# Performance work log

Measured on AMD Instinct MI355X. Metric: run time of the kernel, lower is better.

The kernel has to match this reference:

```python
import jax, jax.numpy as jnp
import numpy as np

N, E, B, L = 500000, 1500000, 64, 512
H, C_IN, C_CONV = 64, 2, 64


def setup_inputs() -> dict:
    key = jax.random.key(0)
    ks = jax.random.split(key, 12)
    x = jax.random.normal(ks[0], (N, C_IN), jnp.float32)
    edge_index = jax.random.randint(ks[1], (2, E), 0, N)
    node_depth = jax.random.randint(ks[2], (N,), 0, L)
    batch_index = jnp.sort(jax.random.randint(ks[3], (N,), 0, B))
    W1 = jax.random.normal(ks[4], (C_IN, H), jnp.float32) / np.sqrt(C_IN)
    b1 = jnp.zeros((H,), jnp.float32)
    W2 = jax.random.normal(ks[5], (H, H), jnp.float32) / np.sqrt(H)
    b2 = jnp.zeros((H,), jnp.float32)
    conv_w = jax.random.normal(ks[6], (C_CONV, 2 * H, 3), jnp.float32) / np.sqrt(2 * H * 3)
    conv_b = jnp.zeros((C_CONV,), jnp.float32)
    fc1_w = jax.random.normal(ks[7], (C_CONV, C_CONV), jnp.float32) / np.sqrt(C_CONV)
    fc1_b = jnp.zeros((C_CONV,), jnp.float32)
    fc2_w = jax.random.normal(ks[8], (C_CONV, 1), jnp.float32) / np.sqrt(C_CONV)
    fc2_b = jnp.zeros((1,), jnp.float32)
    return {"x": x, "edge_index": edge_index, "node_depth": node_depth,
            "batch_index": batch_index, "W1": W1, "b1": b1, "W2": W2, "b2": b2,
            "conv_w": conv_w, "conv_b": conv_b, "fc1_w": fc1_w, "fc1_b": fc1_b,
            "fc2_w": fc2_w, "fc2_b": fc2_b}


def _gcn(x, W, b, src, dst):
    # PyG GCNConv: add self-loops, D^{-1/2} (A+I) D^{-1/2} X W + b
    xw = x @ W
    deg = jnp.zeros((N,), xw.dtype).at[dst].add(1.0) + 1.0  # +1 for self-loop
    dinv = jax.lax.rsqrt(deg)
    norm = dinv[src] * dinv[dst]  # [E]
    agg = jnp.zeros_like(xw).at[dst].add(norm[:, None] * xw[src])
    agg = agg + (dinv * dinv)[:, None] * xw  # self-loop term
    return agg + b


def reference(x, edge_index, node_depth, batch_index, W1, b1, W2, b2,
              conv_w, conv_b, fc1_w, fc1_b, fc2_w, fc2_b):
    src, dst = edge_index[0], edge_index[1]
    h = jax.nn.relu(_gcn(x, W1, b1, src, dst))
    h = jax.nn.relu(_gcn(h, W2, b2, src, dst))

    # LevelWisePool: grouped mean+max keyed by (batch, depth)
    seg = batch_index * L + node_depth  # [N]
    cnt = jax.ops.segment_sum(jnp.ones((N,), h.dtype), seg, num_segments=B * L)
    mean = jax.ops.segment_sum(h, seg, num_segments=B * L) / jnp.maximum(cnt, 1.0)[:, None]
    mx = jax.ops.segment_max(h, seg, num_segments=B * L)
    mx = jnp.where(cnt[:, None] > 0, mx, 0.0)  # empty levels -> zeros
    seq = jnp.concatenate([mean, mx], axis=-1)           # [B*L, 2H]
    seq = seq.reshape(B, L, 2 * H).transpose(0, 2, 1)    # [B, 2H, L]

    y = jax.lax.conv_general_dilated(seq, conv_w, window_strides=(1,),
                                     padding=[(1, 1)],
                                     dimension_numbers=("NCH", "OIH", "NCH"))
    y = jax.nn.relu(y + conv_b[None, :, None])  # [B, C_CONV, L]
    pooled = y.mean(axis=2)                      # [B, C_CONV]

    z = jax.nn.relu(pooled @ fc1_w + fc1_b)
    logits = (z @ fc2_w + fc2_b).reshape(-1)     # [B]
    return jax.nn.sigmoid(logits)
```

## Files before the change

### kernel.cpp

```cpp
#include <hip/hip_runtime.h>

typedef unsigned short ushort_t;
typedef unsigned int uint_t;
typedef __attribute__((ext_vector_type(8))) short short8;
typedef __attribute__((ext_vector_type(4))) float f32x4;

#define NN 500000
#define NE 1500000
#define BATCH 64
#define LSEQ 512
#define NSEG (BATCH * LSEQ)
#define NBLK_E ((NN + 1023) / 1024)
#define NBLK_S (NSEG / 1024)
#define SEQROW 514
#define WPKN (3 * 4 * 4 * 512)
#define PSMASK 0x7FFFFu

__device__ inline float bf2f(ushort_t u) {
    union { uint_t u; float f; } c; c.u = ((uint_t)u) << 16; return c.f;
}
__device__ inline ushort_t f2bf(float f) {
    union { float f; uint_t u; } c; c.f = f;
    uint_t u = c.u;
    return (ushort_t)((u + 0x7fff + ((u >> 16) & 1)) >> 16);
}
__device__ inline int imax(int a, int b) { return a > b ? a : b; }

__global__ void k_zero(float* __restrict__ p, int n) {
    int i = blockIdx.x * blockDim.x + threadIdx.x;
    int stride = gridDim.x * blockDim.x;
    for (; i < n; i += stride) p[i] = 0.0f;
}

__global__ void k_hist2(const int* __restrict__ dst, const int* __restrict__ batch,
                        const int* __restrict__ depth, int* __restrict__ cnt,
                        int* __restrict__ segn, int* __restrict__ cnt2) {
    int t = blockIdx.x * blockDim.x + threadIdx.x;
    if (t < NE) {
        atomicAdd(&cnt[dst[t]], 1);
        if (t < NN) {
            int s = batch[t] * LSEQ + depth[t];
            segn[t] = s;
            atomicAdd(&cnt2[s], 1);
        }
    }
}

__global__ __launch_bounds__(256) void k_scan_block(const int* __restrict__ cnt,
                                                    int* __restrict__ bsum, int n) {
    __shared__ int sd[256];
    int blk = blockIdx.x, tid = threadIdx.x;
    int base = blk * 1024 + tid * 4;
    int s = 0;
#pragma unroll
    for (int k = 0; k < 4; ++k) { int i = base + k; if (i < n) s += cnt[i]; }
    sd[tid] = s;
    __syncthreads();
    for (int off = 128; off; off >>= 1) {
        if (tid < off) sd[tid] += sd[tid + off];
        __syncthreads();
    }
    if (tid == 0) bsum[blk] = sd[0];
}

__global__ __launch_bounds__(512) void k_scan_top(int* __restrict__ bsum, int nblk) {
    __shared__ int sd[512];
    int tid = threadIdx.x;
    int v = (tid < nblk) ? bsum[tid] : 0;
    sd[tid] = v;
    __syncthreads();
    for (int off = 1; off < 512; off <<= 1) {
        int t = (tid >= off) ? sd[tid - off] : 0;
        __syncthreads();
        sd[tid] += t;
        __syncthreads();
    }
    if (tid < nblk) bsum[tid] = sd[tid] - v;
}

__global__ __launch_bounds__(256) void k_scan_final(const int* __restrict__ cnt, const int* __restrict__ bsum,
                                                    int* __restrict__ rowoff, int* __restrict__ cursor,
                                                    int n, int total) {
    __shared__ int sd[256];
    int blk = blockIdx.x, tid = threadIdx.x;
    int base = blk * 1024 + tid * 4;
    int loc[4]; int s = 0;
#pragma unroll
    for (int k = 0; k < 4; ++k) { int i = base + k; int c = (i < n) ? cnt[i] : 0; loc[k] = s; s += c; }
    sd[tid] = s;
    __syncthreads();
    for (int off = 1; off < 256; off <<= 1) {
        int t = (tid >= off) ? sd[tid - off] : 0;
        __syncthreads();
        sd[tid] += t;
        __syncthreads();
    }
    int texc = sd[tid] - s + bsum[blk];
#pragma unroll
    for (int k = 0; k < 4; ++k) {
        int i = base + k;
        if (i < n) { int v = texc + loc[k]; rowoff[i] = v; cursor[i] = v; }
    }
    if (blk == 0 && tid == 0) rowoff[n] = total;
}

__global__ void k_nreorder(const int* __restrict__ segn, int* __restrict__ cursor2,
                           int* __restrict__ nord, int* __restrict__ pos) {
    int n = blockIdx.x * blockDim.x + threadIdx.x;
    if (n >= NN) return;
    int p = atomicAdd(&cursor2[segn[n]], 1);
    nord[p] = n;
    pos[n] = p;
}

__global__ void k_prep(const int* __restrict__ cnt, const int* __restrict__ nord,
                       float* __restrict__ dinvs, int* __restrict__ cntp,
                       const float* __restrict__ x, float2* __restrict__ xs,
                       const float* __restrict__ W2, ushort_t* __restrict__ W2b,
                       const float* __restrict__ cw, ushort_t* __restrict__ wpk) {
    int i = blockIdx.x * blockDim.x + threadIdx.x;
    if (i < NN) {
        int nd = nord[i];
        int dg = cnt[nd];
        cntp[i] = dg;
        float dv = rsqrtf((float)dg + 1.0f);
        dinvs[i] = dv;
        const float2* x2 = (const float2*)x;
        float2 xv = x2[nd];
        xs[i] = make_float2(dv * xv.x, dv * xv.y);
    }
    if (i < 64 * 64) W2b[i] = f2bf(W2[i]);
    if (i < WPKN) {
        int bq = i & 7, ln = (i >> 3) & 63, ct = (i >> 9) & 3, kk = (i >> 11) & 3, tap = i >> 13;
        int c = ct * 16 + (ln & 15);
        int ii = kk * 32 + (ln >> 4) * 8 + bq;
        wpk[i] = f2bf(cw[c * 384 + ii * 3 + tap]);
    }
}

__global__ void k_reorder(const int* __restrict__ src, const int* __restrict__ dst,
                          const int* __restrict__ pos,
                          int* __restrict__ cursor, uint_t* __restrict__ epr) {
    int e = blockIdx.x * blockDim.x + threadIdx.x;
    if (e >= NE) return;
    int ps = pos[src[e]], pd = pos[dst[e]];
    int q = atomicAdd(&cursor[pd], 1);
    epr[q] = (uint_t)ps | ((uint_t)(pd & 15) << 19);
}

__global__ __launch_bounds__(256) void k_build12(const float2* __restrict__ xs,
                                                 const float* __restrict__ W1,
                                                 const float* __restrict__ b1,
                                                 const float* __restrict__ dinvs,
                                                 const int* __restrict__ rowoff,
                                                 const uint_t* __restrict__ epr,
                                                 const ushort_t* __restrict__ W2b,
                                                 ushort_t* __restrict__ xw2) {
    __shared__ float accs[4][32];
    __shared__ ushort_t hl[4][16][64];
    int lane = threadIdx.x & 63;
    int wid = threadIdx.x >> 6;
    int wave = (blockIdx.x * blockDim.x + threadIdx.x) >> 6;
    int nwaves = (gridDim.x * blockDim.x) >> 6;
    int col = lane & 15, kg = lane >> 4;
    float w0 = W1[lane], w1 = W1[64 + lane], bj = b1[lane];
    float* a = accs[wid];
    ushort_t (*h)[64] = hl[wid];
    const float* xsf = (const float*)xs;

    short8 bfrag[2][4];
#pragma unroll
    for (int t = 0; t < 2; ++t)
#pragma unroll
        for (int j = 0; j < 4; ++j)
#pragma unroll
            for (int b = 0; b < 8; ++b) {
                int k = t * 32 + kg * 8 + b;
                bfrag[t][j][b] = (short)W2b[k * 64 + j * 16 + col];
            }

    int kblk = lane >> 3, kin = lane & 7;
    const int NT = NN / 16;
    for (int t = wave; t < NT; t += nwaves) {
        int i0 = t * 16;
        if (lane < 32) a[lane] = xsf[i0 * 2 + lane];
        asm volatile("s_waitcnt lgkmcnt(0)" ::: "memory");
        int e1 = rowoff[i0 + 16];
        for (int e = rowoff[i0] + lane; e < e1; e += 64) {
            uint_t pr = epr[e];
            float2 xv = xs[pr & PSMASK];
            int loc = (pr >> 19) & 15;
            atomicAdd(&a[loc * 2],     xv.x);
            atomicAdd(&a[loc * 2 + 1], xv.y);
        }
        asm volatile("s_waitcnt lgkmcnt(0)" ::: "memory");
#pragma unroll
        for (int j = 0; j < 16; ++j) {
            float dv = dinvs[i0 + j];
            float hv = fmaxf((dv * a[j * 2]) * w0 + (dv * a[j * 2 + 1]) * w1 + bj, 0.0f);
            h[j][((kblk ^ (j & 7)) << 3) + kin] = f2bf(hv);
        }
        asm volatile("s_waitcnt lgkmcnt(0)" ::: "memory");
        short8 a0 = *(const short8*)&h[col][((kg ^ (col & 7)) << 3)];
        short8 a1 = *(const short8*)&h[col][(((kg + 4) ^ (col & 7)) << 3)];
        float dvr[4];
#pragma unroll
        for (int r = 0; r < 4; ++r) dvr[r] = dinvs[i0 + kg * 4 + r];
        size_t base = (size_t)i0 * 64;
        f32x4 acc[4];
#pragma unroll
        for (int j = 0; j < 4; ++j) {
            acc[j] = (f32x4){0.0f, 0.0f, 0.0f, 0.0f};
            acc[j] = __builtin_amdgcn_mfma_f32_16x16x32_bf16(a0, bfrag[0][j], acc[j], 0, 0, 0);
            acc[j] = __builtin_amdgcn_mfma_f32_16x16x32_bf16(a1, bfrag[1][j], acc[j], 0, 0, 0);
        }
#pragma unroll
        for (int j = 0; j < 4; ++j)
#pragma unroll
            for (int r = 0; r < 4; ++r)
                xw2[base + (size_t)(kg * 4 + r) * 64 + j * 16 + col] = f2bf(acc[j][r] * dvr[r]);
    }
}

__global__ __launch_bounds__(256) void k_agg3(const ushort_t* __restrict__ xw2s,
                                              const float* __restrict__ b2,
                                              const float* __restrict__ dinvs,
                                              const int* __restrict__ rowoff,
                                              const uint_t* __restrict__ epr,
                                              ushort_t* __restrict__ aggs) {
    __shared__ float accs[4][16][64];
    int lane = threadIdx.x & 63;
    int wid = threadIdx.x >> 6;
    int wave = (blockIdx.x * blockDim.x + threadIdx.x) >> 6;
    int nwaves = (gridDim.x * blockDim.x) >> 6;
    float bj = b2[lane];
    float (*a)[64] = accs[wid];
    const int NT = NN / 16;
    for (int t = wave; t < NT; t += nwaves) {
        int i0 = t * 16;
#pragma unroll
        for (int j = 0; j < 16; ++j)
            a[j][lane] = bf2f(xw2s[(size_t)(i0 + j) * 64 + lane]);
        int e = rowoff[i0], e1 = rowoff[i0 + 16];
        for (; e + 8 <= e1; e += 8) {
            uint_t p[8];
#pragma unroll
            for (int jj = 0; jj < 8; ++jj) p[jj] = epr[e + jj];
            float v[8];
#pragma unroll
            for (int jj = 0; jj < 8; ++jj)
                v[jj] = bf2f(xw2s[(size_t)(p[jj] & PSMASK) * 64 + lane]);
#pragma unroll
            for (int jj = 0; jj < 8; ++jj)
                a[(p[jj] >> 19) & 15][lane] += v[jj];
        }
        for (; e < e1; ++e) {
            uint_t p = epr[e];
            a[(p >> 19) & 15][lane] += bf2f(xw2s[(size_t)(p & PSMASK) * 64 + lane]);
        }
#pragma unroll
        for (int j = 0; j < 16; ++j) {
            float dv = dinvs[i0 + j];
            aggs[(size_t)(i0 + j) * 64 + lane] = f2bf(fmaxf(dv * a[j][lane] + bj, 0.0f));
        }
    }
}

__global__ __launch_bounds__(256) void k_pool2(const ushort_t* __restrict__ aggs,
                                               const int* __restrict__ soff,
                                               ushort_t* __restrict__ seqb) {
    int lane = threadIdx.x & 63;
    int seg = (blockIdx.x * blockDim.x + threadIdx.x) >> 6;
    if (seg >= NSEG) return;
    int i0 = soff[seg], i1 = soff[seg + 1];
    float ss = 0.0f, sm = 0.0f;
    for (int i = i0; i < i1; ++i) {
        float v = bf2f(aggs[(size_t)i * 64 + lane]);
        ss += v;
        sm = fmaxf(sm, v);
    }
    float mean = ss / fmaxf((float)(i1 - i0), 1.0f);
    size_t row = (size_t)(seg >> 9) * SEQROW + 1 + (seg & 511);
    seqb[row * 128 + lane] = f2bf(mean);
    seqb[row * 128 + 64 + lane] = f2bf(sm);
}

__global__ __launch_bounds__(256) void k_convm(const ushort_t* __restrict__ seqb,
                                               const ushort_t* __restrict__ wpk,
                                               const float* __restrict__ cb,
                                               float* __restrict__ pooled) {
    int lane = threadIdx.x & 63;
    int gw = (blockIdx.x * blockDim.x + threadIdx.x) >> 6;
    int b = gw >> 4;
    int l0base = (gw & 15) * 32;
    int col = lane & 15, kg = lane >> 4;
    float cbv[4];
#pragma unroll
    for (int ct = 0; ct < 4; ++ct) cbv[ct] = cb[ct * 16 + col];
    float csum[4] = {0.0f, 0.0f, 0.0f, 0.0f};
#pragma unroll
    for (int lt = 0; lt < 2; ++lt) {
        int l0 = l0base + lt * 16;
        f32x4 acc[4];
#pragma unroll
        for (int ct = 0; ct < 4; ++ct) acc[ct] = (f32x4){0.0f, 0.0f, 0.0f, 0.0f};
#pragma unroll
        for (int tap = 0; tap < 3; ++tap) {
            size_t row = (size_t)b * SEQROW + l0 + col + tap;
#pragma unroll
            for (int kk = 0; kk < 4; ++kk) {
                short8 av = *(const short8*)(seqb + row * 128 + kk * 32 + kg * 8);
#pragma unroll
                for (int ct = 0; ct < 4; ++ct) {
                    short8 bv = *(const short8*)(wpk + (((tap * 4 + kk) * 4 + ct) << 9) + lane * 8);
                    acc[ct] = __builtin_amdgcn_mfma_f32_16x16x32_bf16(av, bv, acc[ct], 0, 0, 0);
                }
            }
        }
#pragma unroll
        for (int ct = 0; ct < 4; ++ct)
#pragma unroll
            for (int r = 0; r < 4; ++r)
                csum[ct] += fmaxf(acc[ct][r] + cbv[ct], 0.0f);
    }
#pragma unroll
    for (int ct = 0; ct < 4; ++ct) {
        float v = csum[ct];
        v += __shfl_xor(v, 16, 64);
        v += __shfl_xor(v, 32, 64);
        if (lane < 16) atomicAdd(&pooled[b * 64 + ct * 16 + lane], v);
    }
}

__global__ void k_head(const float* __restrict__ pooled, const float* __restrict__ f1w,
                       const float* __restrict__ f1b, const float* __restrict__ f2w,
                       const float* __restrict__ f2b, float* __restrict__ out) {
    int b = blockIdx.x;
    int j = threadIdx.x;
    const float invL = 1.0f / (float)LSEQ;
    float z = f1b[j];
    for (int c = 0; c < 64; ++c)
        z += (pooled[b * 64 + c] * invL) * f1w[c * 64 + j];
    z = fmaxf(z, 0.0f);
    float v = z * f2w[j];
#pragma unroll
    for (int off = 32; off; off >>= 1) v += __shfl_xor(v, off, 64);
    if (j == 0) out[b] = 1.0f / (1.0f + expf(-(v + f2b[0])));
}

extern "C" void kernel_launch(void* const* d_in, const int* in_sizes, int n_in,
                              void* d_out, int out_size, void* d_ws, size_t ws_size,
                              hipStream_t stream) {
    const float* x     = (const float*)d_in[0];
    const int*   ei    = (const int*)d_in[1];
    const int*   depth = (const int*)d_in[2];
    const int*   batch = (const int*)d_in[3];
    const float* W1    = (const float*)d_in[4];
    const float* b1    = (const float*)d_in[5];
    const float* W2    = (const float*)d_in[6];
    const float* b2    = (const float*)d_in[7];
    const float* cw    = (const float*)d_in[8];
    const float* cb    = (const float*)d_in[9];
    const float* f1w   = (const float*)d_in[10];
    const float* f1b   = (const float*)d_in[11];
    const float* f2w   = (const float*)d_in[12];
    const float* f2b   = (const float*)d_in[13];
    float* out = (float*)d_out;

    char* p = (char*)d_ws;
    auto bump = [&p](size_t bytes) { char* r = p; p += (bytes + 15) & ~(size_t)15; return r; };
    int*      cnt    = (int*)bump((size_t)NN * 4);
    int*      cnt2   = (int*)bump((size_t)NSEG * 4);
    float*    pool   = (float*)bump((size_t)BATCH * 64 * 4);
    ushort_t* seqb   = (ushort_t*)bump((size_t)BATCH * SEQROW * 128 * 2);
    int*      segn   = (int*)bump((size_t)NN * 4);
    int*      nord   = (int*)bump((size_t)NN * 4);
    int*      pos    = (int*)bump((size_t)NN * 4);
    int*      soff   = (int*)bump((size_t)(NSEG + 8) * 4);
    int*      cursor2= (int*)bump((size_t)NSEG * 4);
    float*    dinvs  = (float*)bump((size_t)NN * 4);
    float2*   xs     = (float2*)bump((size_t)NN * 8);
    int*      cntp   = (int*)bump((size_t)NN * 4);
    int*      rowoff = (int*)bump((size_t)(NN + 8) * 4);
    int*      cursor = (int*)bump((size_t)NN * 4);
    uint_t*   epr    = (uint_t*)bump((size_t)NE * 4);
    ushort_t* aggs   = (ushort_t*)bump((size_t)NN * 128);
    ushort_t* xw2s   = (ushort_t*)bump((size_t)NN * 128);
    ushort_t* W2b    = (ushort_t*)bump((size_t)64 * 64 * 2);
    ushort_t* wpk    = (ushort_t*)bump((size_t)WPKN * 2);
    int*      bsum   = (int*)bump((size_t)512 * 4);
    int*      bsum2  = (int*)bump((size_t)64 * 4);

    const int* src = ei;
    const int* dst = ei + NE;

    int zn = NN + NSEG + BATCH * 64 + BATCH * SEQROW * 64 + 16;
    k_zero<<<2048, 256, 0, stream>>>((float*)cnt, zn);

    k_hist2<<<(NE + 255) / 256, 256, 0, stream>>>(dst, batch, depth, cnt, segn, cnt2);

    k_scan_block<<<NBLK_S, 256, 0, stream>>>(cnt2, bsum2, NSEG);
    k_scan_top<<<1, 512, 0, stream>>>(bsum2, NBLK_S);
    k_scan_final<<<NBLK_S, 256, 0, stream>>>(cnt2, bsum2, soff, cursor2, NSEG, NN);
    k_nreorder<<<(NN + 255) / 256, 256, 0, stream>>>(segn, cursor2, nord, pos);

    k_prep<<<(NN + 255) / 256, 256, 0, stream>>>(cnt, nord, dinvs, cntp, x, xs, W2, W2b, cw, wpk);

    k_scan_block<<<NBLK_E, 256, 0, stream>>>(cntp, bsum, NN);
    k_scan_top<<<1, 512, 0, stream>>>(bsum, NBLK_E);
    k_scan_final<<<NBLK_E, 256, 0, stream>>>(cntp, bsum, rowoff, cursor, NN, NE);

    k_reorder<<<(NE + 255) / 256, 256, 0, stream>>>(src, dst, pos, cursor, epr);

    k_build12<<<4096, 256, 0, stream>>>(xs, W1, b1, dinvs, rowoff, epr, W2b, xw2s);

    k_agg3<<<4096, 256, 0, stream>>>(xw2s, b2, dinvs, rowoff, epr, aggs);

    k_pool2<<<NSEG / 4, 256, 0, stream>>>(aggs, soff, seqb);

    k_convm<<<256, 256, 0, stream>>>(seqb, wpk, cb, pool);

    k_head<<<BATCH, 64, 0, stream>>>(pool, f1w, f1b, f2w, f2b, out);
}
```

Baseline: 355.4 us.

## Replace edge reorder with two-pass binned scatter for CSR construction

Replaces the single-pass edge reorder, which scattered each edge to a random CSR slot with global atomics, with a two-level counting sort. The first level bins edges into 512-node buckets using per-chunk shared-memory histograms, a column scan and a shared-atomic scatter. The second level places edges within each bucket using global cursor atomics that stay in a small, localized range. The aim is to turn random global atomics and writes into more cache-friendly, localized ones, at the cost of four kernel launches, an extra pass over the edges and an intermediate buffer.

```diff
diff --git a/kernel.cpp b/kernel.cpp
--- a/kernel.cpp
+++ b/kernel.cpp
@@ -15,6 +15,9 @@
 #define SEQROW 514
 #define WPKN (3 * 4 * 4 * 512)
 #define PSMASK 0x7FFFFu
+#define NBIN 977
+#define CHK 2048
+#define NCHK ((NE + CHK - 1) / CHK)
 
 __device__ inline float bf2f(ushort_t u) {
     union { uint_t u; float f; } c; c.u = ((uint_t)u) << 16; return c.f;
@@ -25,6 +28,7 @@
     return (ushort_t)((u + 0x7fff + ((u >> 16) & 1)) >> 16);
 }
 __device__ inline int imax(int a, int b) { return a > b ? a : b; }
+__device__ inline int imin(int a, int b) { return a < b ? a : b; }
 
 __global__ void k_zero(float* __restrict__ p, int n) {
     int i = blockIdx.x * blockDim.x + threadIdx.x;
@@ -138,14 +142,69 @@
     }
 }
 
-__global__ void k_reorder(const int* __restrict__ src, const int* __restrict__ dst,
-                          const int* __restrict__ pos,
-                          int* __restrict__ cursor, uint_t* __restrict__ epr) {
-    int e = blockIdx.x * blockDim.x + threadIdx.x;
-    if (e >= NE) return;
-    int ps = pos[src[e]], pd = pos[dst[e]];
-    int q = atomicAdd(&cursor[pd], 1);
-    epr[q] = (uint_t)ps | ((uint_t)(pd & 15) << 19);
+__global__ __launch_bounds__(256) void k_binh2(const int* __restrict__ dst,
+                                               const int* __restrict__ pos,
+                                               int* __restrict__ histg) {
+    __shared__ int hist[NBIN];
+    int c = blockIdx.x;
+    for (int i = threadIdx.x; i < NBIN; i += 256) hist[i] = 0;
+    __syncthreads();
+    int e0 = c * CHK;
+    for (int k = threadIdx.x; k < CHK; k += 256) {
+        int e = e0 + k;
+        if (e < NE) atomicAdd(&hist[pos[dst[e]] >> 9], 1);
+    }
+    __syncthreads();
+    for (int i = threadIdx.x; i < NBIN; i += 256) histg[c * NBIN + i] = hist[i];
+}
+
+__global__ __launch_bounds__(256) void k_binscan(int* __restrict__ histg,
+                                                 const int* __restrict__ rowoff) {
+    int b = blockIdx.x * 256 + threadIdx.x;
+    if (b >= NBIN) return;
+    int running = rowoff[b << 9];
+    for (int c = 0; c < NCHK; ++c) {
+        int t = histg[c * NBIN + b];
+        histg[c * NBIN + b] = running;
+        running += t;
+    }
+}
+
+__global__ __launch_bounds__(256) void k_scatA2(const int* __restrict__ src,
+                                                const int* __restrict__ dst,
+                                                const int* __restrict__ pos,
+                                                const int* __restrict__ histg,
+                                                uint_t* __restrict__ ebin) {
+    __shared__ int cur[NBIN];
+    int c = blockIdx.x;
+    for (int i = threadIdx.x; i < NBIN; i += 256) cur[i] = histg[c * NBIN + i];
+    __syncthreads();
+    int e0 = c * CHK;
+    for (int k = threadIdx.x; k < CHK; k += 256) {
+        int e = e0 + k;
+        if (e < NE) {
+            int ps = pos[src[e]], pd = pos[dst[e]];
+            int q = atomicAdd(&cur[pd >> 9], 1);
+            ebin[q] = (uint_t)ps | ((uint_t)(pd & 511) << 19);
+        }
+    }
+}
+
+__global__ __launch_bounds__(256) void k_scatB(const uint_t* __restrict__ ebin,
+                                               const int* __restrict__ rowoff,
+                                               int* __restrict__ cursor,
+                                               uint_t* __restrict__ epr) {
+    int b = blockIdx.x;
+    int e0 = rowoff[b << 9];
+    int e1 = rowoff[imin((b + 1) << 9, NN)];
+    int base = b << 9;
+    for (int i = e0 + threadIdx.x; i < e1; i += 256) {
+        uint_t r = ebin[i];
+        int relpd = (int)((r >> 19) & 511);
+        int pd = base + relpd;
+        int q = atomicAdd(&cursor[pd], 1);
+        epr[q] = (r & PSMASK) | ((uint_t)(relpd & 15) << 19);
+    }
 }
 
 __global__ __launch_bounds__(256) void k_build12(const float2* __restrict__ xs,
@@ -384,6 +443,8 @@
     int*      rowoff = (int*)bump((size_t)(NN + 8) * 4);
     int*      cursor = (int*)bump((size_t)NN * 4);
     uint_t*   epr    = (uint_t*)bump((size_t)NE * 4);
+    uint_t*   ebin   = (uint_t*)bump((size_t)NE * 4);
+    int*      histg  = (int*)bump((size_t)NCHK * NBIN * 4);
     ushort_t* aggs   = (ushort_t*)bump((size_t)NN * 128);
     ushort_t* xw2s   = (ushort_t*)bump((size_t)NN * 128);
     ushort_t* W2b    = (ushort_t*)bump((size_t)64 * 64 * 2);
@@ -410,7 +471,10 @@
     k_scan_top<<<1, 512, 0, stream>>>(bsum, NBLK_E);
     k_scan_final<<<NBLK_E, 256, 0, stream>>>(cntp, bsum, rowoff, cursor, NN, NE);
 
-    k_reorder<<<(NE + 255) / 256, 256, 0, stream>>>(src, dst, pos, cursor, epr);
+    k_binh2<<<NCHK, 256, 0, stream>>>(dst, pos, histg);
+    k_binscan<<<(NBIN + 255) / 256, 256, 0, stream>>>(histg, rowoff);
+    k_scatA2<<<NCHK, 256, 0, stream>>>(src, dst, pos, histg, ebin);
+    k_scatB<<<NBIN, 256, 0, stream>>>(ebin, rowoff, cursor, epr);
 
     k_build12<<<4096, 256, 0, stream>>>(xs, W1, b1, dinvs, rowoff, epr, W2b, xw2s);
 
```

After: 407.2 us. 14.6% more time.

## Build CSR via two-pass binned counting sort instead of global atomics

Applied to the files above, without the earlier changes.

Replaces the global-atomic degree histogram, full-length exclusive scan and atomic scatter with a two-level bucket sort. Edges are first binned into 4096-node buckets using per-chunk LDS histograms, then each bucket is sorted locally in shared memory. The local sort also produces row offsets and degree normalisation. This aims to cut contended global atomics and random writes, at the cost of more kernel launches and an extra pass over the edges through an intermediate buffer.

```diff
diff --git a/kernel.cpp b/kernel.cpp
--- a/kernel.cpp
+++ b/kernel.cpp
@@ -10,11 +10,15 @@
 #define BATCH 64
 #define LSEQ 512
 #define NSEG (BATCH * LSEQ)
-#define NBLK_E ((NN + 1023) / 1024)
 #define NBLK_S (NSEG / 1024)
 #define SEQROW 514
 #define WPKN (3 * 4 * 4 * 512)
 #define PSMASK 0x7FFFFu
+#define BSH 12
+#define BSZ 4096
+#define NBIN2 ((NN + BSZ - 1) / BSZ)
+#define NCHK2 256
+#define CHK2 ((NE + NCHK2 - 1) / NCHK2)
 
 __device__ inline float bf2f(ushort_t u) {
     union { uint_t u; float f; } c; c.u = ((uint_t)u) << 16; return c.f;
@@ -24,7 +28,7 @@
     uint_t u = c.u;
     return (ushort_t)((u + 0x7fff + ((u >> 16) & 1)) >> 16);
 }
-__device__ inline int imax(int a, int b) { return a > b ? a : b; }
+__device__ inline int imin(int a, int b) { return a < b ? a : b; }
 
 __global__ void k_zero(float* __restrict__ p, int n) {
     int i = blockIdx.x * blockDim.x + threadIdx.x;
@@ -32,17 +36,13 @@
     for (; i < n; i += stride) p[i] = 0.0f;
 }
 
-__global__ void k_hist2(const int* __restrict__ dst, const int* __restrict__ batch,
-                        const int* __restrict__ depth, int* __restrict__ cnt,
-                        int* __restrict__ segn, int* __restrict__ cnt2) {
-    int t = blockIdx.x * blockDim.x + threadIdx.x;
-    if (t < NE) {
-        atomicAdd(&cnt[dst[t]], 1);
-        if (t < NN) {
-            int s = batch[t] * LSEQ + depth[t];
-            segn[t] = s;
-            atomicAdd(&cnt2[s], 1);
-        }
+__global__ void k_seg(const int* __restrict__ batch, const int* __restrict__ depth,
+                      int* __restrict__ segn, int* __restrict__ cnt2) {
+    int n = blockIdx.x * blockDim.x + threadIdx.x;
+    if (n < NN) {
+        int s = batch[n] * LSEQ + depth[n];
+        segn[n] = s;
+        atomicAdd(&cnt2[s], 1);
     }
 }
 
@@ -113,22 +113,9 @@
     pos[n] = p;
 }
 
-__global__ void k_prep(const int* __restrict__ cnt, const int* __restrict__ nord,
-                       float* __restrict__ dinvs, int* __restrict__ cntp,
-                       const float* __restrict__ x, float2* __restrict__ xs,
-                       const float* __restrict__ W2, ushort_t* __restrict__ W2b,
-                       const float* __restrict__ cw, ushort_t* __restrict__ wpk) {
+__global__ void k_prepW(const float* __restrict__ W2, ushort_t* __restrict__ W2b,
+                        const float* __restrict__ cw, ushort_t* __restrict__ wpk) {
     int i = blockIdx.x * blockDim.x + threadIdx.x;
-    if (i < NN) {
-        int nd = nord[i];
-        int dg = cnt[nd];
-        cntp[i] = dg;
-        float dv = rsqrtf((float)dg + 1.0f);
-        dinvs[i] = dv;
-        const float2* x2 = (const float2*)x;
-        float2 xv = x2[nd];
-        xs[i] = make_float2(dv * xv.x, dv * xv.y);
-    }
     if (i < 64 * 64) W2b[i] = f2bf(W2[i]);
     if (i < WPKN) {
         int bq = i & 7, ln = (i >> 3) & 63, ct = (i >> 9) & 3, kk = (i >> 11) & 3, tap = i >> 13;
@@ -138,14 +125,133 @@
     }
 }
 
-__global__ void k_reorder(const int* __restrict__ src, const int* __restrict__ dst,
-                          const int* __restrict__ pos,
-                          int* __restrict__ cursor, uint_t* __restrict__ epr) {
-    int e = blockIdx.x * blockDim.x + threadIdx.x;
-    if (e >= NE) return;
-    int ps = pos[src[e]], pd = pos[dst[e]];
-    int q = atomicAdd(&cursor[pd], 1);
-    epr[q] = (uint_t)ps | ((uint_t)(pd & 15) << 19);
+__global__ void k_prepx(const float* __restrict__ x, const int* __restrict__ nord,
+                        const float* __restrict__ dinvs, float2* __restrict__ xs) {
+    int i = blockIdx.x * blockDim.x + threadIdx.x;
+    if (i >= NN) return;
+    float dv = dinvs[i];
+    const float2* x2 = (const float2*)x;
+    float2 xv = x2[nord[i]];
+    xs[i] = make_float2(dv * xv.x, dv * xv.y);
+}
+
+__global__ __launch_bounds__(256) void k_binh2(const int* __restrict__ dst,
+                                               const int* __restrict__ pos,
+                                               int* __restrict__ histg) {
+    __shared__ int hist[NBIN2];
+    int c = blockIdx.x;
+    for (int i = threadIdx.x; i < NBIN2; i += 256) hist[i] = 0;
+    __syncthreads();
+    int e0 = c * CHK2, e1 = imin(e0 + CHK2, NE);
+    for (int e = e0 + threadIdx.x; e < e1; e += 256)
+        atomicAdd(&hist[pos[dst[e]] >> BSH], 1);
+    __syncthreads();
+    for (int i = threadIdx.x; i < NBIN2; i += 256) histg[c * NBIN2 + i] = hist[i];
+}
+
+__global__ __launch_bounds__(64) void k_binT(const int* __restrict__ histg, int* __restrict__ T) {
+    int b = blockIdx.x, lane = threadIdx.x;
+    int s = 0;
+    for (int c = lane; c < NCHK2; c += 64) s += histg[c * NBIN2 + b];
+#pragma unroll
+    for (int off = 32; off; off >>= 1) s += __shfl_down(s, off, 64);
+    if (lane == 0) T[b] = s;
+}
+
+__global__ __launch_bounds__(128) void k_boff(const int* __restrict__ T, int* __restrict__ boff) {
+    __shared__ int sd[128];
+    int t = threadIdx.x;
+    int v = (t < NBIN2) ? T[t] : 0;
+    sd[t] = v;
+    __syncthreads();
+    for (int off = 1; off < 128; off <<= 1) {
+        int y = (t >= off) ? sd[t - off] : 0;
+        __syncthreads();
+        sd[t] += y;
+        __syncthreads();
+    }
+    if (t < NBIN2) boff[t] = sd[t] - v;
+    if (t == 0) boff[NBIN2] = NE;
+}
+
+__global__ __launch_bounds__(64) void k_binbase(int* __restrict__ histg, const int* __restrict__ boff) {
+    int b = blockIdx.x, lane = threadIdx.x;
+    int h[4]; int s = 0;
+#pragma unroll
+    for (int k = 0; k < 4; ++k) h[k] = histg[(lane * 4 + k) * NBIN2 + b];
+#pragma unroll
+    for (int k = 0; k < 4; ++k) { int pre = s; s += h[k]; h[k] = pre; }
+    int x = s;
+    for (int d = 1; d < 64; d <<= 1) { int y = __shfl_up(x, d, 64); if (lane >= d) x += y; }
+    int base = x - s + boff[b];
+#pragma unroll
+    for (int k = 0; k < 4; ++k) histg[(lane * 4 + k) * NBIN2 + b] = base + h[k];
+}
+
+__global__ __launch_bounds__(256) void k_scatA2(const int* __restrict__ src,
+                                                const int* __restrict__ dst,
+                                                const int* __restrict__ pos,
+                                                const int* __restrict__ histg,
+                                                uint_t* __restrict__ ebin) {
+    __shared__ int cur[NBIN2];
+    int c = blockIdx.x;
+    for (int i = threadIdx.x; i < NBIN2; i += 256) cur[i] = histg[c * NBIN2 + i];
+    __syncthreads();
+    int e0 = c * CHK2, e1 = imin(e0 + CHK2, NE);
+    for (int e = e0 + threadIdx.x; e < e1; e += 256) {
+        int ps = pos[src[e]], pd = pos[dst[e]];
+        int q = atomicAdd(&cur[pd >> BSH], 1);
+        ebin[q] = (uint_t)ps | ((uint_t)(pd & (BSZ - 1)) << 19);
+    }
+}
+
+__global__ __launch_bounds__(256) void k_binsort(const uint_t* __restrict__ ebin,
+                                                 const int* __restrict__ boff,
+                                                 uint_t* __restrict__ epr,
+                                                 int* __restrict__ rowoff,
+                                                 float* __restrict__ dinvs) {
+    __shared__ int lh[BSZ];
+    __shared__ int sd[256];
+    int b = blockIdx.x, tid = threadIdx.x;
+    for (int j = tid; j < BSZ; j += 256) lh[j] = 0;
+    __syncthreads();
+    int e0 = boff[b], e1 = boff[b + 1];
+    for (int i = e0 + tid; i < e1; i += 256)
+        atomicAdd(&lh[(ebin[i] >> 19) & (BSZ - 1)], 1);
+    __syncthreads();
+    int cnt16[16]; int s = 0;
+    int base16 = tid * 16;
+#pragma unroll
+    for (int k = 0; k < 16; ++k) { cnt16[k] = lh[base16 + k]; s += cnt16[k]; }
+    sd[tid] = s;
+    __syncthreads();
+    for (int off = 1; off < 256; off <<= 1) {
+        int y = (tid >= off) ? sd[tid - off] : 0;
+        __syncthreads();
+        sd[tid] += y;
+        __syncthreads();
+    }
+    int run = sd[tid] - s;
+    int gbase = b << BSH;
+#pragma unroll
+    for (int k = 0; k < 16; ++k) {
+        int j = base16 + k;
+        int g = gbase + j;
+        if (g < NN) {
+            rowoff[g] = e0 + run;
+            dinvs[g] = rsqrtf((float)cnt16[k] + 1.0f);
+        }
+        lh[j] = run;
+        run += cnt16[k];
+    }
+    if (b == NBIN2 - 1 && tid == 0) rowoff[NN] = NE;
+    __syncthreads();
+    for (int i = e0 + tid; i < e1; i += 256) {
+        uint_t r = ebin[i];
+        int rel = (r >> 19) & (BSZ - 1);
+        int q = e0 + atomicAdd(&lh[rel], 1);
+        epr[q] = (r & PSMASK) | ((uint_t)(rel & 15) << 19);
+    }
 }
 
 __global__ __launch_bounds__(256) void k_build12(const float2* __restrict__ xs,
@@ -369,7 +475,6 @@
 
     char* p = (char*)d_ws;
     auto bump = [&p](size_t bytes) { char* r = p; p += (bytes + 15) & ~(size_t)15; return r; };
-    int*      cnt    = (int*)bump((size_t)NN * 4);
     int*      cnt2   = (int*)bump((size_t)NSEG * 4);
     float*    pool   = (float*)bump((size_t)BATCH * 64 * 4);
     ushort_t* seqb   = (ushort_t*)bump((size_t)BATCH * SEQROW * 128 * 2);
@@ -380,37 +485,40 @@
     int*      cursor2= (int*)bump((size_t)NSEG * 4);
     float*    dinvs  = (float*)bump((size_t)NN * 4);
     float2*   xs     = (float2*)bump((size_t)NN * 8);
-    int*      cntp   = (int*)bump((size_t)NN * 4);
     int*      rowoff = (int*)bump((size_t)(NN + 8) * 4);
-    int*      cursor = (int*)bump((size_t)NN * 4);
     uint_t*   epr    = (uint_t*)bump((size_t)NE * 4);
+    uint_t*   ebin   = (uint_t*)bump((size_t)NE * 4);
+    int*      histg  = (int*)bump((size_t)NCHK2 * NBIN2 * 4);
+    int*      Tb     = (int*)bump((size_t)(NBIN2 + 8) * 4);
+    int*      boff   = (int*)bump((size_t)(NBIN2 + 8) * 4);
     ushort_t* aggs   = (ushort_t*)bump((size_t)NN * 128);
     ushort_t* xw2s   = (ushort_t*)bump((size_t)NN * 128);
     ushort_t* W2b    = (ushort_t*)bump((size_t)64 * 64 * 2);
     ushort_t* wpk    = (ushort_t*)bump((size_t)WPKN * 2);
-    int*      bsum   = (int*)bump((size_t)512 * 4);
     int*      bsum2  = (int*)bump((size_t)64 * 4);
 
     const int* src = ei;
     const int* dst = ei + NE;
 
-    int zn = NN + NSEG + BATCH * 64 + BATCH * SEQROW * 64 + 16;
-    k_zero<<<2048, 256, 0, stream>>>((float*)cnt, zn);
-
-    k_hist2<<<(NE + 255) / 256, 256, 0, stream>>>(dst, batch, depth, cnt, segn, cnt2);
-
+    int zn = NSEG + BATCH * 64 + BATCH * SEQROW * 64 + 16;
+    k_zero<<<2048, 256, 0, stream>>>((float*)cnt2, zn);
+
+    k_seg<<<(NN + 255) / 256, 256, 0, stream>>>(batch, depth, segn, cnt2);
     k_scan_block<<<NBLK_S, 256, 0, stream>>>(cnt2, bsum2, NSEG);
     k_scan_top<<<1, 512, 0, stream>>>(bsum2, NBLK_S);
     k_scan_final<<<NBLK_S, 256, 0, stream>>>(cnt2, bsum2, soff, cursor2, NSEG, NN);
     k_nreorder<<<(NN + 255) / 256, 256, 0, stream>>>(segn, cursor2, nord, pos);
 
-    k_prep<<<(NN + 255) / 256, 256, 0, stream>>>(cnt, nord, dinvs, cntp, x, xs, W2, W2b, cw, wpk);
-
-    k_scan_block<<<NBLK_E, 256, 0, stream>>>(cntp, bsum, NN);
-    k_scan_top<<<1, 512, 0, stream>>>(bsum, NBLK_E);
-    k_scan_final<<<NBLK_E, 256, 0, stream>>>(cntp, bsum, rowoff, cursor, NN, NE);
-
-    k_reorder<<<(NE + 255) / 256, 256, 0, stream>>>(src, dst, pos, cursor, epr);
+    k_prepW<<<(WPKN + 255) / 256, 256, 0, stream>>>(W2, W2b, cw, wpk);
+
+    k_binh2<<<NCHK2, 256, 0, stream>>>(dst, pos, histg);
+    k_binT<<<NBIN2, 64, 0, stream>>>(histg, Tb);
+    k_boff<<<1, 128, 0, stream>>>(Tb, boff);
+    k_binbase<<<NBIN2, 64, 0, stream>>>(histg, boff);
+    k_scatA2<<<NCHK2, 256, 0, stream>>>(src, dst, pos, histg, ebin);
+    k_binsort<<<NBIN2, 256, 0, stream>>>(ebin, boff, epr, rowoff, dinvs);
+
+    k_prepx<<<(NN + 255) / 256, 256, 0, stream>>>(x, nord, dinvs, xs);
 
     k_build12<<<4096, 256, 0, stream>>>(xs, W1, b1, dinvs, rowoff, epr, W2b, xw2s);
 
```

Result: faster. 292.5 us (-17.7%).
